# Performance work log

Hardware: AMD Instinct MI355X
Metric: run time of the kernel (lower is better)

## Reference

```python
import jax, jax.numpy as jnp
import numpy as np

N_WG = 512      # waveguides n
N_COL = 512     # mesh columns
M = N_WG // 2   # node slots per column (odd columns have one masked dummy)
N_NODE = N_COL * M
B = 8192        # batch of input fields
PI4 = np.pi / 4


def build_mesh_indices():
    """Rectangular (Clements-style) mesh: per-column (top, bottom, mask) arrays."""
    top = np.zeros((N_COL, M), np.int32)
    bottom = np.zeros((N_COL, M), np.int32)
    mask = np.zeros((N_COL, M), np.int32)
    for c in range(N_COL):
        if c % 2 == 0:
            t = np.arange(0, N_WG, 2, dtype=np.int32)
            top[c], bottom[c], mask[c] = t, t + 1, 1
        else:
            t = np.arange(1, N_WG - 1, 2, dtype=np.int32)
            k = len(t)
            top[c, :k], bottom[c, :k], mask[c, :k] = t, t + 1, 1
            # masked dummy slot uses otherwise-unused rows 0 and N_WG-1
            top[c, k:], bottom[c, k:] = 0, N_WG - 1
    return jnp.asarray(top), jnp.asarray(bottom), jnp.asarray(mask)


def setup_inputs() -> dict:
    key = jax.random.key(0)
    ks = jax.random.split(key, 6)
    top, bottom, mask = build_mesh_indices()
    return {
        "x": jax.random.normal(ks[0], (N_WG, B), dtype=jnp.float32),
        "thetas": 2 * np.pi * jax.random.uniform(ks[1], (N_NODE,), dtype=jnp.float32),
        "phis": 2 * np.pi * jax.random.uniform(ks[2], (N_NODE,), dtype=jnp.float32),
        "gammas": 2 * np.pi * jax.random.uniform(ks[3], (N_WG,), dtype=jnp.float32),
        "bs_errors": 0.01 * jax.random.normal(ks[4], (N_NODE, 2), dtype=jnp.float32),
        "loss_errors": -0.1 * jax.random.uniform(ks[5], (N_NODE, 2), dtype=jnp.float32),
        "top": top, "bottom": bottom, "mask": mask,
    }


def _dc_terms(bs_errors, loss_errors, side):
    """_parallel_dc: per-node directional-coupler 2x2 elements [N,4] complex."""
    ins = jnp.exp(jnp.log(10.0) * loss_errors[:, side] / 20.0)
    e = bs_errors[:, side]
    s, c = jnp.sin(PI4 + e), jnp.cos(PI4 + e)
    t11 = (ins * s).astype(jnp.complex64)
    t12 = ins * (1j * c)
    t21 = (1j * c).astype(jnp.complex64)
    t22 = s.astype(jnp.complex64)
    return jnp.stack([t11, t12, t21, t22], axis=-1)


def _transform(v, T, t, b, m):
    """_parallel_transform: masked 2x2 gather-multiply-scatter. T: [M,4] complex."""
    vt, vb = v[t], v[b]
    one_m = 1.0 - m
    s11 = (T[:, 0] * m + one_m)[:, None]
    s12 = (T[:, 1] * m)[:, None]
    s21 = (T[:, 2] * m)[:, None]
    s22 = (T[:, 3] * m + one_m)[:, None]
    return v.at[t].set(s11 * vt + s21 * vb).at[b].set(s12 * vt + s22 * vb)


def reference(x, thetas, phis, gammas, bs_errors, loss_errors, top, bottom, mask):
    # input gamma phase screen, then propagate through all mesh columns
    v = x.astype(jnp.complex64) * jnp.exp(1j * gammas)[:, None]          # [n, B]
    left = _dc_terms(bs_errors, loss_errors, 0).reshape(N_COL, M, 4)
    right = _dc_terms(bs_errors, loss_errors, 1).reshape(N_COL, M, 4)
    th = thetas.reshape(N_COL, M)
    ph = phis.reshape(N_COL, M)
    mf = mask.astype(jnp.float32)

    def column(v, xs):
        t, b, m, thc, phc, L, R = xs
        # PhaseStyle.TOP, forward: phi -> left DC -> theta -> right DC
        v = v.at[t].multiply(jnp.exp(1j * phc * m)[:, None])
        v = _transform(v, L, t, b, m)
        v = v.at[t].multiply(jnp.exp(1j * thc * m)[:, None])
        v = _transform(v, R, t, b, m)
        return v, None

    v, _ = jax.lax.scan(column, v, (top, bottom, mf, th, ph, left, right))
    return jnp.stack([v.real, v.imag])  # [2, n, B]
```

## Files before the change

### kernel.cpp

```cpp
#include <hip/hip_runtime.h>
#include <math.h>

#define BATCH 8192
#define NROW 512
#define NCOL 512
#define MNODE 256

typedef __attribute__((ext_vector_type(8))) short bf16x8;
typedef __attribute__((ext_vector_type(4))) float f32x4;

__device__ __forceinline__ short2 split1(float x) {
  unsigned u = __float_as_uint(x);
  short h = (short)(u >> 16);
  float r = x - __uint_as_float(u & 0xffff0000u);
  short l = (short)(__float_as_uint(r) >> 16);
  return make_short2(h, l);
}

__global__ __launch_bounds__(256) void precomp_kernel(
    const float* __restrict__ thetas, const float* __restrict__ phis,
    const float* __restrict__ bse, const float* __restrict__ lse,
    float4* __restrict__ pp) {
  int n = blockIdx.x * 256 + threadIdx.x;
  float th = thetas[n], ph = phis[n];
  float e0 = bse[2 * n + 0], e1 = bse[2 * n + 1];
  float l0 = lse[2 * n + 0], l1 = lse[2 * n + 1];
  const float K = 0.16609640474436813f;
  float ins0 = exp2f(l0 * K), ins1 = exp2f(l1 * K);
  const float PI4 = 0.7853981633974483f;
  float s0, c0, s1, c1, sp, cp, st, ct;
  sincosf(PI4 + e0, &s0, &c0);
  sincosf(PI4 + e1, &s1, &c1);
  sincosf(ph, &sp, &cp);
  sincosf(th, &st, &ct);
  float AL = ins0 * s0, C1L = c0, C2L = ins0 * c0, SL = s0;
  float AR = ins1 * s1, C1R = c1, C2R = ins1 * c1, SR = s1;
  float a11r = AL * cp,   a11i = AL * sp;
  float a12r = 0.f,       a12i = C1L;
  float a21r = -C2L * sp, a21i = C2L * cp;
  float a22r = SL,        a22i = 0.f;
  float b11r = a11r * ct - a11i * st, b11i = a11r * st + a11i * ct;
  float b12r = a12r * ct - a12i * st, b12i = a12r * st + a12i * ct;
  float n11r = AR * b11r - C1R * a21i;
  float n11i = AR * b11i + C1R * a21r;
  float n12r = AR * b12r - C1R * a22i;
  float n12i = AR * b12i + C1R * a22r;
  float n21r = -C2R * b11i + SR * a21r;
  float n21i =  C2R * b11r + SR * a21i;
  float n22r = -C2R * b12i + SR * a22r;
  float n22i =  C2R * b12r + SR * a22i;
  pp[2 * n + 0] = make_float4(n11r, n11i, n12r, n12i);
  pp[2 * n + 1] = make_float4(n21r, n21i, n22r, n22i);
}

__device__ __forceinline__ void proc_pair(float& vtr, float& vti, float& vbr, float& vbi,
                                          const float4 q0, const float4 q1) {
  float tr = q0.x * vtr - q0.y * vti + q0.z * vbr - q0.w * vbi;
  float ti = q0.x * vti + q0.y * vtr + q0.z * vbi + q0.w * vbr;
  float br = q1.x * vtr - q1.y * vti + q1.z * vbr - q1.w * vbi;
  float bi = q1.x * vti + q1.y * vtr + q1.z * vbi + q1.w * vbr;
  vtr = tr; vti = ti; vbr = br; vbi = bi;
}

__device__ __forceinline__ int swz(int b) { return b ^ ((b >> 3) & 7); }

__global__ __launch_bounds__(256) void compose_kernel(
    const float* __restrict__ gammas, const float4* __restrict__ pp,
    float* __restrict__ Tsegs, int pairs_per_seg) {
  __shared__ float4 buf[2][1024];
  float* epf = (float*)buf;

  const int tid  = threadIdx.x;
  const int lane = tid & 63;
  const int w    = tid >> 6;
  const int seg  = blockIdx.x >> 7;
  const int g    = blockIdx.x & 127;
  const int col  = g * 4 + w;
  const int colmin = g * 4;

  const float4* ps = pp + (size_t)seg * pairs_per_seg * 1024;
  float* T = Tsegs + (size_t)seg * (1024 * NROW);

  float vr[8], vi[8];
#pragma unroll
  for (int r = 0; r < 8; ++r) {
    const int row = lane * 8 + r;
    vr[r] = 0.f; vi[r] = 0.f;
    if (row == col) {
      if (seg == 0) {
        float sg, cg;
        sincosf(gammas[row], &sg, &cg);
        vr[r] = cg; vi[r] = sg;
      } else {
        vr[r] = 1.f;
      }
    }
  }

  {
    const int sw = swz(tid);
#pragma unroll
    for (int k = 0; k < 4; ++k)
      buf[0][256 * k + sw] = ps[256 * k + tid];
  }
  __syncthreads();

  const int Lc = col >> 3;

#pragma unroll 1
  for (int p = 0; p < pairs_per_seg; ++p) {
    const int b = p & 1;

    const int HA = (p >> 2) + 3;
    const bool act  = (lane >= Lc - HA)     && (lane <= Lc + HA);
    const bool wide = (lane >= Lc - HA - 1) && (lane <= Lc + HA + 1);

    float4 f0, f1, f2, f3;
    bool st0 = false, st1 = false;
    if (p < pairs_per_seg - 1) {
      const int slo = colmin - 2 * p - 50;
      const int shi = colmin + 2 * p + 53;
      st0 = (tid + 1 >= slo) && (tid <= shi);
      st1 = (tid + 257 >= slo) && (tid + 256 <= shi);
      const float4* src = ps + (size_t)(p + 1) * 1024;
      if (st0) { f0 = src[tid];       f2 = src[512 + tid]; }
      if (st1) { f1 = src[256 + tid]; f3 = src[768 + tid]; }
    }

    float4 pe[8], po[7], pu1;
    if (act) {
      const int base = 8 * lane;
      const int l7 = lane & 7;
#pragma unroll
      for (int j = 0; j < 8; ++j) pe[j] = buf[b][base + (j ^ l7)];
#pragma unroll
      for (int j = 0; j < 7; ++j) po[j] = buf[b][512 + base + (j ^ l7)];
      const int lm = (lane == 0) ? 0 : lane - 1;
      pu1 = buf[b][512 + 8 * lm + (7 ^ (lm & 7))];

#pragma unroll
      for (int k = 0; k < 4; ++k)
        proc_pair(vr[2 * k], vi[2 * k], vr[2 * k + 1], vi[2 * k + 1],
                  pe[2 * k], pe[2 * k + 1]);

#pragma unroll
      for (int k = 0; k < 3; ++k)
        proc_pair(vr[2 * k + 1], vi[2 * k + 1], vr[2 * k + 2], vi[2 * k + 2],
                  po[2 * k], po[2 * k + 1]);
    }

    float br = 0.f, bi = 0.f, tu = 0.f, tv = 0.f;
    if (wide) {
      br = __shfl_down(vr[0], 1, 64);
      bi = __shfl_down(vi[0], 1, 64);
      tu = __shfl_up(vr[7], 1, 64);
      tv = __shfl_up(vi[7], 1, 64);
    }
    if (act) {
      float nAr = po[6].x * vr[7] - po[6].y * vi[7] + po[6].z * br - po[6].w * bi;
      float nAi = po[6].x * vi[7] + po[6].y * vr[7] + po[6].z * bi + po[6].w * br;
      float nBr = pu1.x * tu - pu1.y * tv + pu1.z * vr[0] - pu1.w * vi[0];
      float nBi = pu1.x * tv + pu1.y * tu + pu1.z * vi[0] + pu1.w * vr[0];
      if (lane < 63) { vr[7] = nAr; vi[7] = nAi; }
      if (lane > 0)  { vr[0] = nBr; vi[0] = nBi; }
    }

    if (p < pairs_per_seg - 1) {
      const int sw = swz(tid);
      if (st0) { buf[1 - b][sw] = f0;       buf[1 - b][512 + sw] = f2; }
      if (st1) { buf[1 - b][256 + sw] = f1; buf[1 - b][768 + sw] = f3; }
    }
    __syncthreads();
  }

#pragma unroll
  for (int r = 0; r < 8; ++r) {
    epf[(lane * 8 + r) * 5 + w] = vr[r];
    epf[(512 + lane * 8 + r) * 5 + w] = vi[r];
  }
  __syncthreads();
#pragma unroll
  for (int k = 0; k < 4; ++k) {
    const int i = k * 256 + tid;
    *(float4*)(T + (size_t)i * NROW + g * 4) =
        make_float4(epf[i * 5 + 0], epf[i * 5 + 1], epf[i * 5 + 2], epf[i * 5 + 3]);
  }
}

__global__ __launch_bounds__(256) void merge_g(
    const float* __restrict__ Ab, const float* __restrict__ Bb,
    float* __restrict__ Cb, long sA, long sB, long sC, int HA, int HB) {
  const float* A = Ab + (long)blockIdx.z * sA;
  const float* B = Bb + (long)blockIdx.z * sB;
  float*       C = Cb + (long)blockIdx.z * sC;

  __shared__ short sAh[64 * 40], sAl[64 * 40];

  const int tid = threadIdx.x;
  const int lane = tid & 63;
  const int w = tid >> 6;
  const int bm = blockIdx.y * 64;
  const int bn = blockIdx.x * 64;
  const int wm = (w & 1) * 32;
  const int wn = (w >> 1) * 32;
  const int q = lane >> 4;
  const int l15 = lane & 15;

  const int sm = tid >> 2;
  const int sk = (tid & 3) * 8;

  const int rmin = (blockIdx.y & 7) * 64;
  int klo = rmin - HA;
  {
    int t = bn - HB;
    if (t > klo) klo = t;
    if (klo < 0) klo = 0;
  }
  int khi = rmin + 63 + HA;
  {
    int t = bn + 63 + HB;
    if (t < khi) khi = t;
    if (khi > 511) khi = 511;
  }
  klo &= ~31;

  f32x4 acc[2][2];
#pragma unroll
  for (int i = 0; i < 2; ++i)
#pragma unroll
    for (int j = 0; j < 2; ++j) acc[i][j] = (f32x4){0.f, 0.f, 0.f, 0.f};

  if (klo <= khi) {
#pragma unroll 1
    for (int h = 0; h < 2; ++h) {
#pragma unroll 1
      for (int k0 = klo; k0 <= khi; k0 += 32) {
        const int gkb = h * 512 + k0;
        {
          const int gm = bm + sm;
          const int gk = gkb + sk;
          const int r = gm & 511;
          const bool top = gm < 512;
          const bool left = gk < 512;
          const int col = gk & 511;
          const float* src = (top == left) ? (A + (size_t)r * 512)
                                           : (A + (size_t)(512 + r) * 512);
          const float sgn = (top && !left) ? -1.f : 1.f;
          float4 v0 = *(const float4*)(src + col);
          float4 v1 = *(const float4*)(src + col + 4);
          float vv[8] = {v0.x, v0.y, v0.z, v0.w, v1.x, v1.y, v1.z, v1.w};
          short hh[8], ll[8];
#pragma unroll
          for (int i = 0; i < 8; ++i) {
            short2 s = split1(sgn * vv[i]);
            hh[i] = s.x; ll[i] = s.y;
          }
          __syncthreads();
          *(bf16x8*)&sAh[sm * 40 + sk] = *(bf16x8*)hh;
          *(bf16x8*)&sAl[sm * 40 + sk] = *(bf16x8*)ll;
          __syncthreads();
        }

        bf16x8 bh[2], bl[2];
#pragma unroll
        for (int nt = 0; nt < 2; ++nt) {
          const float* bp = B + (size_t)(gkb + q * 8) * 512 + bn + wn + nt * 16 + l15;
          short hh[8], ll[8];
#pragma unroll
          for (int j = 0; j < 8; ++j) {
            short2 s = split1(bp[(size_t)j * 512]);
            hh[j] = s.x; ll[j] = s.y;
          }
          bh[nt] = *(bf16x8*)hh;
          bl[nt] = *(bf16x8*)ll;
        }

        bf16x8 ah[2], al[2];
#pragma unroll
        for (int mt = 0; mt < 2; ++mt) {
          const int m = wm + mt * 16 + l15;
          ah[mt] = *(const bf16x8*)&sAh[m * 40 + q * 8];
          al[mt] = *(const bf16x8*)&sAl[m * 40 + q * 8];
        }

#pragma unroll
        for (int mt = 0; mt < 2; ++mt)
#pragma unroll
          for (int nt = 0; nt < 2; ++nt) {
            acc[mt][nt] = __builtin_amdgcn_mfma_f32_16x16x32_bf16(ah[mt], bh[nt], acc[mt][nt], 0, 0, 0);
            acc[mt][nt] = __builtin_amdgcn_mfma_f32_16x16x32_bf16(ah[mt], bl[nt], acc[mt][nt], 0, 0, 0);
            acc[mt][nt] = __builtin_amdgcn_mfma_f32_16x16x32_bf16(al[mt], bh[nt], acc[mt][nt], 0, 0, 0);
          }
      }
    }
  }

#pragma unroll
  for (int mt = 0; mt < 2; ++mt)
#pragma unroll
    for (int nt = 0; nt < 2; ++nt)
#pragma unroll
      for (int r = 0; r < 4; ++r) {
        const int gm = bm + wm + mt * 16 + q * 4 + r;
        const int gn = bn + wn + nt * 16 + l15;
        C[(size_t)gm * 512 + gn] = acc[mt][nt][r];
      }
}

__global__ __launch_bounds__(256) void xprep_kernel(
    const float* __restrict__ x, short* __restrict__ xp) {
  const int t = blockIdx.x * 256 + threadIdx.x;
  const int n = t & 8191;
  const int g = t >> 13;
  const float* src = x + (size_t)g * 8 * BATCH + n;
  short h[8], l[8];
#pragma unroll
  for (int j = 0; j < 8; ++j) {
    short2 s = split1(src[(size_t)j * BATCH]);
    h[j] = s.x; l[j] = s.y;
  }
  short* dst = xp + (size_t)t * 16;
  *(bf16x8*)dst = *(bf16x8*)h;
  *(bf16x8*)(dst + 8) = *(bf16x8*)l;
}

__global__ __launch_bounds__(256) void gemm_mfma_packed(
    const float* __restrict__ A, const short* __restrict__ xp,
    float* __restrict__ C) {
  __shared__ short sAh[64 * 40], sAl[64 * 40];

  const int tid = threadIdx.x;
  const int lane = tid & 63;
  const int w = tid >> 6;
  const int bm = blockIdx.y * 64;
  const int bn = blockIdx.x * 128;
  const int wm = (w & 1) * 32;
  const int wn = (w >> 1) * 64;
  const int q = lane >> 4;
  const int l15 = lane & 15;

  const int sm = tid >> 2;
  const int sk = (tid & 3) * 8;
  const float* Ap = A + (size_t)(bm + sm) * 512 + sk;

  f32x4 acc[2][4];
#pragma unroll
  for (int i = 0; i < 2; ++i)
#pragma unroll
    for (int j = 0; j < 4; ++j) acc[i][j] = (f32x4){0.f, 0.f, 0.f, 0.f};

  float4 pa[2];
  pa[0] = *(const float4*)(Ap);
  pa[1] = *(const float4*)(Ap + 4);

#pragma unroll 1
  for (int k0 = 0; k0 < 512; k0 += 32) {
    {
      short h[8], l[8];
#pragma unroll
      for (int i = 0; i < 8; ++i) {
        short2 s = split1(((const float*)pa)[i]);
        h[i] = s.x; l[i] = s.y;
      }
      __syncthreads();
      *(bf16x8*)&sAh[sm * 40 + sk] = *(bf16x8*)h;
      *(bf16x8*)&sAl[sm * 40 + sk] = *(bf16x8*)l;
      __syncthreads();
    }

    if (k0 + 32 < 512) {
      pa[0] = *(const float4*)(Ap + k0 + 32);
      pa[1] = *(const float4*)(Ap + k0 + 36);
    }

    const int kt = k0 >> 5;
    bf16x8 bh[4], bl[4];
#pragma unroll
    for (int nt = 0; nt < 4; ++nt) {
      const short* bp = xp + (((size_t)(kt * 4 + q)) * BATCH +
                              (bn + wn + nt * 16 + l15)) * 16;
      bh[nt] = *(const bf16x8*)bp;
      bl[nt] = *(const bf16x8*)(bp + 8);
    }

    bf16x8 ah[2], al[2];
#pragma unroll
    for (int mt = 0; mt < 2; ++mt) {
      const int m = wm + mt * 16 + l15;
      ah[mt] = *(const bf16x8*)&sAh[m * 40 + q * 8];
      al[mt] = *(const bf16x8*)&sAl[m * 40 + q * 8];
    }

#pragma unroll
    for (int mt = 0; mt < 2; ++mt)
#pragma unroll
      for (int nt = 0; nt < 4; ++nt) {
        acc[mt][nt] = __builtin_amdgcn_mfma_f32_16x16x32_bf16(ah[mt], bh[nt], acc[mt][nt], 0, 0, 0);
        acc[mt][nt] = __builtin_amdgcn_mfma_f32_16x16x32_bf16(ah[mt], bl[nt], acc[mt][nt], 0, 0, 0);
        acc[mt][nt] = __builtin_amdgcn_mfma_f32_16x16x32_bf16(al[mt], bh[nt], acc[mt][nt], 0, 0, 0);
      }
  }

#pragma unroll
  for (int mt = 0; mt < 2; ++mt)
#pragma unroll
    for (int nt = 0; nt < 4; ++nt)
#pragma unroll
      for (int r = 0; r < 4; ++r) {
        const int gm = bm + wm + mt * 16 + q * 4 + r;
        const int gn = bn + wn + nt * 16 + l15;
        C[(size_t)gm * BATCH + gn] = acc[mt][nt][r];
      }
}

__global__ __launch_bounds__(256) void gemm_mfma(
    const float* __restrict__ A, const float* __restrict__ B,
    float* __restrict__ C) {
  __shared__ short sAh[128 * 40], sAl[128 * 40];

  const int tid = threadIdx.x;
  const int lane = tid & 63;
  const int w = tid >> 6;
  const int bm = blockIdx.y * 128;
  const int bn = blockIdx.x * 128;
  const int wm = (w & 1) * 64;
  const int wn = (w >> 1) * 64;
  const int q = lane >> 4;
  const int l15 = lane & 15;

  const int sm = tid >> 1;
  const int sk = (tid & 1) * 16;
  const float* Ap = A + (size_t)(bm + sm) * 512 + sk;

  f32x4 acc[4][4];
#pragma unroll
  for (int i = 0; i < 4; ++i)
#pragma unroll
    for (int j = 0; j < 4; ++j) acc[i][j] = (f32x4){0.f, 0.f, 0.f, 0.f};

  float4 pa[4];
#pragma unroll
  for (int i = 0; i < 4; ++i) pa[i] = *(const float4*)(Ap + i * 4);

#pragma unroll 1
  for (int k0 = 0; k0 < 512; k0 += 32) {
    {
      short h[16], l[16];
#pragma unroll
      for (int i = 0; i < 16; ++i) {
        short2 s = split1(((const float*)pa)[i]);
        h[i] = s.x; l[i] = s.y;
      }
      __syncthreads();
      *(bf16x8*)&sAh[sm * 40 + sk]     = *(bf16x8*)&h[0];
      *(bf16x8*)&sAh[sm * 40 + sk + 8] = *(bf16x8*)&h[8];
      *(bf16x8*)&sAl[sm * 40 + sk]     = *(bf16x8*)&l[0];
      *(bf16x8*)&sAl[sm * 40 + sk + 8] = *(bf16x8*)&l[8];
      __syncthreads();
    }

    if (k0 + 32 < 512) {
#pragma unroll
      for (int i = 0; i < 4; ++i) pa[i] = *(const float4*)(Ap + k0 + 32 + i * 4);
    }

    bf16x8 bh[4], bl[4];
#pragma unroll
    for (int nt = 0; nt < 4; ++nt) {
      const float* bp = B + (size_t)(k0 + q * 8) * BATCH + bn + wn + nt * 16 + l15;
      short hh[8], ll[8];
#pragma unroll
      for (int j = 0; j < 8; ++j) {
        short2 s = split1(bp[(size_t)j * BATCH]);
        hh[j] = s.x; ll[j] = s.y;
      }
      bh[nt] = *(bf16x8*)hh;
      bl[nt] = *(bf16x8*)ll;
    }

    bf16x8 ah[4], al[4];
#pragma unroll
    for (int mt = 0; mt < 4; ++mt) {
      const int m = wm + mt * 16 + l15;
      ah[mt] = *(const bf16x8*)&sAh[m * 40 + q * 8];
      al[mt] = *(const bf16x8*)&sAl[m * 40 + q * 8];
    }

#pragma unroll
    for (int mt = 0; mt < 4; ++mt)
#pragma unroll
      for (int nt = 0; nt < 4; ++nt) {
        acc[mt][nt] = __builtin_amdgcn_mfma_f32_16x16x32_bf16(ah[mt], bh[nt], acc[mt][nt], 0, 0, 0);
        acc[mt][nt] = __builtin_amdgcn_mfma_f32_16x16x32_bf16(ah[mt], bl[nt], acc[mt][nt], 0, 0, 0);
        acc[mt][nt] = __builtin_amdgcn_mfma_f32_16x16x32_bf16(al[mt], bh[nt], acc[mt][nt], 0, 0, 0);
      }
  }

#pragma unroll
  for (int mt = 0; mt < 4; ++mt)
#pragma unroll
    for (int nt = 0; nt < 4; ++nt)
#pragma unroll
      for (int r = 0; r < 4; ++r) {
        const int gm = bm + wm + mt * 16 + q * 4 + r;
        const int gn = bn + wn + nt * 16 + l15;
        C[(size_t)gm * BATCH + gn] = acc[mt][nt][r];
      }
}

extern "C" void kernel_launch(void* const* d_in, const int* in_sizes, int n_in,
                              void* d_out, int out_size, void* d_ws, size_t ws_size,
                              hipStream_t stream) {
  const float* x      = (const float*)d_in[0];
  const float* thetas = (const float*)d_in[1];
  const float* phis   = (const float*)d_in[2];
  const float* gammas = (const float*)d_in[3];
  const float* bse    = (const float*)d_in[4];
  const float* lse    = (const float*)d_in[5];

  float* base = (float*)d_ws;
  float4* pp  = (float4*)d_ws;
  const long PPF   = 1048576;
  const long S     = 524288;

  precomp_kernel<<<512, 256, 0, stream>>>(thetas, phis, bse, lse, pp);

  if (ws_size >= (size_t)24 * 1024 * 1024) {
    float* segs = base + PPF;
    compose_kernel<<<1024, 256, 0, stream>>>(gammas, pp, segs, 32);

    float* U0 = base + 5 * PPF;
    float* U1 = base + 5 * PPF + S;
    float* U2 = base;
    float* U3 = base + S;
    merge_g<<<dim3(8, 16, 2), 256, 0, stream>>>(
        segs + S, segs, U0, 2 * S, 2 * S, S, 68, 68);
    merge_g<<<dim3(8, 16, 2), 256, 0, stream>>>(
        segs + 5 * S, segs + 4 * S, U2, 2 * S, 2 * S, S, 68, 68);
    float* V0 = base + PPF;
    float* V1 = base + PPF + S;
    merge_g<<<dim3(8, 16, 2), 256, 0, stream>>>(
        U1, U0, V0, (long)(U3 - U1), (long)(U2 - U0), S, 136, 136);
    float* Tf = base;
    merge_g<<<dim3(8, 16, 1), 256, 0, stream>>>(V1, V0, Tf, 0, 0, 0, 272, 272);

    short* xp = (short*)(base + S);
    xprep_kernel<<<2048, 256, 0, stream>>>(x, xp);

    gemm_mfma_packed<<<dim3(64, 16), 256, 0, stream>>>(Tf, xp, (float*)d_out);
  } else {
    int nseg;
    if (ws_size >= (size_t)14 * 1024 * 1024)      nseg = 4;
    else if (ws_size >= (size_t)8 * 1024 * 1024)  nseg = 2;
    else                                          nseg = 1;

    float* segs = base + PPF;
    float* Tf;
    compose_kernel<<<nseg * 128, 256, 0, stream>>>(gammas, pp, segs, 256 / nseg);

    if (nseg == 4) {
      float* T10 = base;
      float* T32 = base + S;
      Tf = segs + 4 * S;
      merge_g<<<dim3(8, 16, 2), 256, 0, stream>>>(
          segs + S, segs, T10, 2 * S, 2 * S, S, 132, 132);
      merge_g<<<dim3(8, 16, 1), 256, 0, stream>>>(
          T32, T10, Tf, 0, 0, 0, 264, 264);
    } else if (nseg == 2) {
      Tf = base;
      merge_g<<<dim3(8, 16, 1), 256, 0, stream>>>(
          segs + S, segs, Tf, 0, 0, 0, 260, 260);
    } else {
      Tf = segs;
    }

    gemm_mfma<<<dim3(BATCH / 128, 8), 256, 0, stream>>>(Tf, x, (float*)d_out);
  }
}
```

Before: 262.8 us.

## Replace segment compose kernel with banded per-wavefront light-cone composition

Adds compose_band, which builds each segment's transfer-matrix column by tracking only the 128-row band (light cone) reachable from the source waveguide within 32 column pairs. Each lane holds one even/odd row pair in registers and exchanges neighbours with wavefront shuffles instead of propagating the full 512-row vector through shared memory. This is meant to cut arithmetic and LDS traffic in the compose stage. In exchange it needs edge-case handling for the spill row at the band boundary, and it relies on the segment length staying at 32 pairs so the band fits in one wavefront.

```diff
diff --git a/kernel.cpp b/kernel.cpp
--- a/kernel.cpp
+++ b/kernel.cpp
@@ -64,6 +64,123 @@
 
 __device__ __forceinline__ int swz(int b) { return b ^ ((b >> 3) & 7); }
 
+__global__ __launch_bounds__(256) void compose_band(
+    const float* __restrict__ gammas, const float4* __restrict__ pp,
+    float* __restrict__ Tsegs, int P) {
+  __shared__ float ep[5120];
+
+  const int tid  = threadIdx.x;
+  const int lane = tid & 63;
+  const int w    = tid >> 6;
+  const int seg  = blockIdx.x >> 7;
+  const int g    = blockIdx.x & 127;
+  const int col  = g * 4 + w;
+
+  const float4* ps = pp + (size_t)seg * P * 1024;
+  float* T = Tsegs + (size_t)seg * (1024 * NROW);
+
+  const int colA = (col - 63) & ~1;
+  const int E    = colA + 2 * lane;
+  const int je   = E >> 1;
+  const int jeC  = je < 0 ? 0 : (je > 255 ? 255 : je);
+
+  const bool vE  = (E >= 0) && (E <= 510);
+  const bool vOT = (E >= 0) && (E <= 508);
+  const bool vOB = (E >= 2) && (E <= 510);
+
+  float ar = 0.f, ai = 0.f, br = 0.f, bi = 0.f;
+  {
+    float vr0 = 1.f, vi0 = 0.f;
+    if (seg == 0) {
+      float sg, cg;
+      sincosf(gammas[col], &sg, &cg);
+      vr0 = cg; vi0 = sg;
+    }
+    if (E == col)     { ar = vr0; ai = vi0; }
+    if (E + 1 == col) { br = vr0; bi = vi0; }
+  }
+
+  const float4* pe = ps + 2 * jeC;
+  const float4* po = ps + 512 + 2 * jeC;
+
+  float sar = 0.f, sai = 0.f, sbr = 0.f, sbi = 0.f;
+
+  for (int p = 0; p < P; ++p) {
+    float4 q0 = pe[0];
+    float4 q1 = pe[1];
+    float4 o0 = po[0];
+    float4 o1 = po[-1];
+    pe += 1024; po += 1024;
+
+    {
+      float tr = q0.x * ar - q0.y * ai + q0.z * br - q0.w * bi;
+      float ti = q0.x * ai + q0.y * ar + q0.z * bi + q0.w * br;
+      float ur = q1.x * ar - q1.y * ai + q1.z * br - q1.w * bi;
+      float ui = q1.x * ai + q1.y * ar + q1.z * bi + q1.w * br;
+      if (vE) { ar = tr; ai = ti; br = ur; bi = ui; }
+    }
+
+    if (p == P - 1) { sar = ar; sai = ai; sbr = br; sbi = bi; }
+
+    float anr = __shfl_down(ar, 1, 64);
+    float ani = __shfl_down(ai, 1, 64);
+    float bpr = __shfl_up(br, 1, 64);
+    float bpi = __shfl_up(bi, 1, 64);
+    if (lane == 63) { anr = 0.f; ani = 0.f; }
+    if (lane == 0)  { bpr = 0.f; bpi = 0.f; }
+    {
+      float tr = o0.x * br - o0.y * bi + o0.z * anr - o0.w * ani;
+      float ti = o0.x * bi + o0.y * br + o0.z * ani + o0.w * anr;
+      float ur = o1.x * bpr - o1.y * bpi + o1.z * ar - o1.w * ai;
+      float ui = o1.x * bpi + o1.y * bpr + o1.z * ai + o1.w * ar;
+      if (vOT) { br = tr; bi = ti; }
+      if (vOB) { ar = ur; ai = ui; }
+    }
+  }
+
+  int sprow = -1;
+  float spr = 0.f, spi = 0.f;
+  if ((col & 1) == 0) {
+    if (colA + 128 <= 511) {
+      sprow = colA + 128;
+      float4 w1 = ps[(size_t)(P - 1) * 1024 + 512 + 2 * (colA / 2 + 63) + 1];
+      float vtr = __shfl(sbr, 63, 64);
+      float vti = __shfl(sbi, 63, 64);
+      spr = w1.x * vtr - w1.y * vti;
+      spi = w1.x * vti + w1.y * vtr;
+    }
+  } else {
+    if (colA - 1 >= 0) {
+      sprow = colA - 1;
+      float4 w0 = ps[(size_t)(P - 1) * 1024 + 512 + 2 * (colA / 2 - 1)];
+      float vbr = __shfl(sar, 0, 64);
+      float vbi = __shfl(sai, 0, 64);
+      spr = w0.z * vbr - w0.w * vbi;
+      spi = w0.z * vbi + w0.w * vbr;
+    }
+  }
+
+  for (int i = tid; i < 5120; i += 256) ep[i] = 0.f;
+  __syncthreads();
+  if (E >= 0 && E <= 510) {
+    ep[E * 5 + w]         = ar;
+    ep[(512 + E) * 5 + w] = ai;
+    ep[(E + 1) * 5 + w]       = br;
+    ep[(513 + E) * 5 + w]     = bi;
+  }
+  if (lane == 0 && sprow >= 0) {
+    ep[sprow * 5 + w]         = spr;
+    ep[(512 + sprow) * 5 + w] = spi;
+  }
+  __syncthreads();
+#pragma unroll
+  for (int k = 0; k < 4; ++k) {
+    const int i = k * 256 + tid;
+    *(float4*)(T + (size_t)i * NROW + g * 4) =
+        make_float4(ep[i * 5 + 0], ep[i * 5 + 1], ep[i * 5 + 2], ep[i * 5 + 3]);
+  }
+}
+
 __global__ __launch_bounds__(256) void compose_kernel(
     const float* __restrict__ gammas, const float4* __restrict__ pp,
     float* __restrict__ Tsegs, int pairs_per_seg) {
@@ -527,7 +644,7 @@
 
   if (ws_size >= (size_t)24 * 1024 * 1024) {
     float* segs = base + PPF;
-    compose_kernel<<<1024, 256, 0, stream>>>(gammas, pp, segs, 32);
+    compose_band<<<1024, 256, 0, stream>>>(gammas, pp, segs, 32);
 
     float* U0 = base + 5 * PPF;
     float* U1 = base + 5 * PPF + S;
```

New measurement: 227.0 us. -13.6%, faster.
